# Performance work log

Measured on AMD Instinct MI355X. Metric: run time of the kernel, lower is better.

The kernel has to match this reference:

```python
import jax, jax.numpy as jnp
import numpy as np

C = 256
C8 = C // 8


def setup_inputs() -> dict:
    key = jax.random.key(0)
    ks = jax.random.split(key, 8)
    B, H, W = 4, 64, 64
    s = 0.05
    return {
        "x": jax.random.normal(ks[0], (B, C, H, W), jnp.float32),
        "Wq": jax.random.normal(ks[1], (C8, C), jnp.float32) * s,
        "bq": jax.random.normal(ks[2], (C8,), jnp.float32) * s,
        "Wk": jax.random.normal(ks[3], (C8, C), jnp.float32) * s,
        "bk": jax.random.normal(ks[4], (C8,), jnp.float32) * s,
        "Wv": jax.random.normal(ks[5], (C, C), jnp.float32) * s,
        "bv": jax.random.normal(ks[6], (C,), jnp.float32) * s,
        "gamma": jnp.zeros((1,), jnp.float32),
    }


def reference(x, Wq, bq, Wk, bk, Wv, bv, gamma):
    B, Ch, H, W = x.shape
    N = H * W
    xf = x.reshape(B, Ch, N)  # [B,C,N]
    # 1x1 convs == channel-mixing matmuls
    q = jnp.einsum("oc,bcn->bon", Wq, xf) + bq[None, :, None]  # [B,C8,N]
    k = jnp.einsum("oc,bcn->bon", Wk, xf) + bk[None, :, None]  # [B,C8,N]
    v = jnp.einsum("oc,bcn->bon", Wv, xf) + bv[None, :, None]  # [B,C,N]
    # energy[b,i,j] = sum_c q[b,c,i] * k[b,c,j]  (unscaled, as in original)
    energy = jnp.einsum("bci,bcj->bij", q, k)  # [B,N,N]
    attention = jax.nn.softmax(energy, axis=-1)  # softmax over j
    # out[b,c,i] = sum_j v[b,c,j] * attention[b,i,j]
    out = jnp.einsum("bcj,bij->bci", v, attention).reshape(B, Ch, H, W)
    out = gamma[0] * out + x
    attention_map = attention[0]
    return out, attention_map
```

## Files before the change

kernel.cpp:

```cpp
#include <hip/hip_runtime.h>
#include <hip/hip_bf16.h>
#include <cstdint>
#include <cstddef>

#define C_    256
#define C8_   32
#define NPIX  4096
#define BATCH 4
#define OUT_ELEMS (BATCH * C_ * NPIX)

typedef short bf16x8 __attribute__((ext_vector_type(8)));
typedef float f32x4  __attribute__((ext_vector_type(4)));
typedef unsigned uint32x2 __attribute__((ext_vector_type(2)));

#define LOG2E 1.44269504088896340736f

#define PROW 520

static __device__ __forceinline__ unsigned short f2bf(float f) {
    union { float f; unsigned u; } v; v.f = f;
    unsigned r = v.u + 0x7fff + ((v.u >> 16) & 1);
    return (unsigned short)(r >> 16);
}

static __device__ __forceinline__ unsigned pack_bf2(float p0, float p1) {
    union { float f; unsigned u; } a, b; a.f = p0; b.f = p1;
    return __builtin_amdgcn_perm(b.u, a.u, 0x07060302u);
}
static __device__ __forceinline__ float unpk_lo(unsigned u) {
    union { unsigned u; float f; } v; v.u = u << 16; return v.f;
}
static __device__ __forceinline__ float unpk_hi(unsigned u) {
    union { unsigned u; float f; } v; v.u = u & 0xffff0000u; return v.f;
}

static __device__ __forceinline__ f32x4 mfma16(bf16x8 a, bf16x8 b, f32x4 c) {
    return __builtin_amdgcn_mfma_f32_16x16x32_bf16(a, b, c, 0, 0, 0);
}

__global__ __launch_bounds__(256) void k_pre(
    const float* __restrict__ x,
    const float* __restrict__ Wq, const float* __restrict__ bq,
    const float* __restrict__ Wk, const float* __restrict__ bk,
    const float* __restrict__ Wv, const float* __restrict__ bv,
    const float* __restrict__ gamma,
    float* __restrict__ out,
    unsigned short* __restrict__ qT,
    unsigned short* __restrict__ kT,
    unsigned short* __restrict__ vB)
{
    __shared__ float xs[256][64];
    __shared__ float pred[4][8][64];

    const int bid = blockIdx.x;
    const float gval = gamma[0];

    if (bid >= 2048) {
        const size_t base = (size_t)(bid - 2048) * 256 + threadIdx.x;
        const f32x4* src = (const f32x4*)x;
        f32x4* dst = (f32x4*)out;
        f32x4 a = src[base];
        f32x4 b = src[base + 524288];
        __builtin_nontemporal_store(a, dst + base);
        __builtin_nontemporal_store(b, dst + base + 524288);
        return;
    }

    const int b   = bid >> 9;
    if (gval == 0.0f && b > 0) return;
    const int sub  = bid & 511;
    const int og8  = sub >> 6;
    const int n0   = (sub & 63) * 64;
    const bool is_q = (og8 < 4);
    const int obase = (og8 & 3) * 8;

    const int tl = threadIdx.x & 15;
    const int tr = threadIdx.x >> 4;
    const float* xb = x + (size_t)b * C_ * NPIX + n0;
    f32x4 v[16];
#pragma unroll
    for (int p = 0; p < 16; ++p)
        v[p] = *(const f32x4*)(xb + (size_t)(p * 16 + tr) * NPIX + tl * 4);
#pragma unroll
    for (int p = 0; p < 16; ++p)
        *(f32x4*)&xs[p * 16 + tr][tl * 4] = v[p];
    __syncthreads();

    const int wv = __builtin_amdgcn_readfirstlane(threadIdx.x >> 6);
    const int ln = threadIdx.x & 63;
    const float* Wb = (is_q ? Wq : Wk);
    float acc[8] = {0.f, 0.f, 0.f, 0.f, 0.f, 0.f, 0.f, 0.f};
#pragma unroll 8
    for (int cc = 0; cc < 64; ++cc) {
        const int c = wv * 64 + cc;
        const float xv = xs[c][ln];
#pragma unroll
        for (int o = 0; o < 8; ++o)
            acc[o] = fmaf(Wb[(size_t)(obase + o) * C_ + c], xv, acc[o]);
    }
#pragma unroll
    for (int o = 0; o < 8; ++o) pred[wv][o][ln] = acc[o];
    __syncthreads();

    const int o1 = threadIdx.x >> 6;
    const int n  = threadIdx.x & 63;
#pragma unroll
    for (int k = 0; k < 2; ++k) {
        const int ol = o1 + k * 4;
        const int oa = obase + ol;
        float s = pred[0][ol][n] + pred[1][ol][n] +
                  pred[2][ol][n] + pred[3][ol][n];
        if (is_q) {
            s = (s + bq[oa]) * LOG2E;
            qT[((size_t)b * NPIX + n0 + n) * C8_ + oa] = f2bf(s);
        } else {
            s = s + bk[oa];
            kT[((size_t)b * NPIX + n0 + n) * C8_ + oa] = f2bf(s);
        }
    }

    if (gval != 0.0f) {
        for (int ch = 0; ch < 4; ++ch) {
            const int vb0 = og8 * 32 + ch * 8;
            float vacc[8] = {0.f, 0.f, 0.f, 0.f, 0.f, 0.f, 0.f, 0.f};
#pragma unroll 8
            for (int cc = 0; cc < 64; ++cc) {
                const int c = wv * 64 + cc;
                const float xv = xs[c][ln];
#pragma unroll
                for (int o = 0; o < 8; ++o)
                    vacc[o] = fmaf(Wv[(size_t)(vb0 + o) * C_ + c], xv, vacc[o]);
            }
            __syncthreads();
#pragma unroll
            for (int o = 0; o < 8; ++o) pred[wv][o][ln] = vacc[o];
            __syncthreads();
#pragma unroll
            for (int k = 0; k < 2; ++k) {
                const int ol = o1 + k * 4;
                const int oa = vb0 + ol;
                float s = pred[0][ol][n] + pred[1][ol][n] +
                          pred[2][ol][n] + pred[3][ol][n] + bv[oa];
                vB[((size_t)b * C_ + oa) * NPIX + n0 + n] = f2bf(s);
            }
        }
    }
}

__global__ __launch_bounds__(512) void k_attn6(
    const float* __restrict__ x,
    const unsigned short* __restrict__ qT,
    const unsigned short* __restrict__ kT,
    const unsigned short* __restrict__ vB,
    const float* __restrict__ gamma,
    float* __restrict__ out,
    float* __restrict__ attn)
{
    const int b = blockIdx.y;
    const float g = gamma[0];
    if (g == 0.0f && b > 0) return;

    const int i0   = blockIdx.x * 16;
    const int t    = threadIdx.x;
    const int lane = t & 63;
    const int wavei = __builtin_amdgcn_readfirstlane(t >> 6);
    const int li   = lane & 15;
    const int lg   = lane >> 4;

    __shared__ unsigned short pbuf[8 * 16 * PROW];
    __shared__ float red[8][16];

    const unsigned short* qTb = qT + (size_t)b * NPIX * C8_;
    const unsigned short* kTb = kT + (size_t)b * NPIX * C8_;

    bf16x8 qf = *(const bf16x8*)(qTb + (size_t)(i0 + li) * C8_ + lg * 8);

    const int jw = wavei * 512;
    unsigned short* prow = pbuf + (size_t)(wavei * 16 + li) * PROW;

    float ssum = 0.f;
#pragma unroll
    for (int s = 0; s < 32; ++s) {
        bf16x8 kf = *(const bf16x8*)(kTb + (size_t)(jw + s * 16 + li) * C8_ + lg * 8);
        f32x4 z = {0.f, 0.f, 0.f, 0.f};
        f32x4 e = mfma16(kf, qf, z);
        float p0 = exp2f(e[0]);
        float p1 = exp2f(e[1]);
        float p2 = exp2f(e[2]);
        float p3 = exp2f(e[3]);
        ssum += (p0 + p1) + (p2 + p3);
        uint32x2 pk;
        pk.x = pack_bf2(p0, p1);
        pk.y = pack_bf2(p2, p3);
        *(uint32x2*)(prow + s * 16 + lg * 4) = pk;
    }

    ssum += __shfl_xor(ssum, 16, 64);
    ssum += __shfl_xor(ssum, 32, 64);
    if (lane < 16) red[wavei][lane] = ssum;
    __syncthreads();
    float l = 0.f;
#pragma unroll
    for (int w = 0; w < 8; ++w) l += red[w][li];
    const float inv = 1.0f / l;

    if (b == 0) {
#pragma unroll
        for (int r = 0; r < 16; ++r) {
            const float inv_r = __shfl(inv, r, 64);
            const unsigned short* rp = pbuf + (size_t)(wavei * 16 + r) * PROW;
            float* ap = attn + (size_t)(i0 + r) * NPIX + jw;
            uint32x2 u0 = *(const uint32x2*)(rp + lane * 4);
            uint32x2 u1 = *(const uint32x2*)(rp + 256 + lane * 4);
            f32x4 v0, v1;
            v0[0] = unpk_lo(u0.x) * inv_r; v0[1] = unpk_hi(u0.x) * inv_r;
            v0[2] = unpk_lo(u0.y) * inv_r; v0[3] = unpk_hi(u0.y) * inv_r;
            v1[0] = unpk_lo(u1.x) * inv_r; v1[1] = unpk_hi(u1.x) * inv_r;
            v1[2] = unpk_lo(u1.y) * inv_r; v1[3] = unpk_hi(u1.y) * inv_r;
            __builtin_nontemporal_store(v0, (f32x4*)(ap + lane * 4));
            __builtin_nontemporal_store(v1, (f32x4*)(ap + 256 + lane * 4));
        }
    }

    if (g != 0.0f) {
        f32x4 o0 = {0.f, 0.f, 0.f, 0.f};
        f32x4 o1 = {0.f, 0.f, 0.f, 0.f};
        const unsigned short* vb = vB + (size_t)b * C_ * NPIX;
        for (int st = 0; st < 8; ++st) {
            const int jbase = st * 512;
#pragma unroll
            for (int ks = 0; ks < 16; ++ks) {
                bf16x8 af = *(const bf16x8*)(pbuf + (size_t)(st * 16 + li) * PROW +
                                             ks * 32 + lg * 8);
                const unsigned short* vp0 =
                    vb + (size_t)(wavei * 32 + li) * NPIX + jbase + ks * 32 + lg * 8;
                bf16x8 vf0 = *(const bf16x8*)vp0;
                o0 = mfma16(af, vf0, o0);
                bf16x8 vf1 = *(const bf16x8*)(vp0 + (size_t)16 * NPIX);
                o1 = mfma16(af, vf1, o1);
            }
        }
        const float* xbt = x + (size_t)b * C_ * NPIX;
        float* outb = out + (size_t)b * C_ * NPIX;
        f32x4 sc;
#pragma unroll
        for (int r = 0; r < 4; ++r) sc[r] = g * __shfl(inv, lg * 4 + r, 64);
        {
            int c = wavei * 32 + li;
            f32x4 xv = *(const f32x4*)(xbt + (size_t)c * NPIX + i0 + lg * 4);
            f32x4 r0 = o0 * sc + xv;
            *(f32x4*)(outb + (size_t)c * NPIX + i0 + lg * 4) = r0;
            c += 16;
            f32x4 xv1 = *(const f32x4*)(xbt + (size_t)c * NPIX + i0 + lg * 4);
            f32x4 r1 = o1 * sc + xv1;
            *(f32x4*)(outb + (size_t)c * NPIX + i0 + lg * 4) = r1;
        }
    }
}

extern "C" void kernel_launch(void* const* d_in, const int* in_sizes, int n_in,
                              void* d_out, int out_size, void* d_ws, size_t ws_size,
                              hipStream_t stream) {
    (void)in_sizes; (void)n_in; (void)out_size; (void)ws_size;
    const float* x     = (const float*)d_in[0];
    const float* Wq    = (const float*)d_in[1];
    const float* bq    = (const float*)d_in[2];
    const float* Wk    = (const float*)d_in[3];
    const float* bk    = (const float*)d_in[4];
    const float* Wv    = (const float*)d_in[5];
    const float* bv    = (const float*)d_in[6];
    const float* gamma = (const float*)d_in[7];

    float* out  = (float*)d_out;
    float* attn = out + OUT_ELEMS;

    unsigned short* qT = (unsigned short*)d_ws;
    unsigned short* kT = qT + (size_t)BATCH * NPIX * C8_;
    unsigned short* vB = kT + (size_t)BATCH * NPIX * C8_;

    k_pre<<<4096, 256, 0, stream>>>(x, Wq, bq, Wk, bk, Wv, bv, gamma,
                                    out, qT, kT, vB);

    dim3 g2(NPIX / 16, BATCH);
    k_attn6<<<g2, 512, 0, stream>>>(x, qT, kT, vB, gamma, out, attn);
}
```

Before: 34.75 us.

## Move output copy into idle attention blocks and write full attention rows per wave

The x-to-out residual copy is removed from the preprocessing kernel. Attention blocks for batches 1-3, which exit early when gamma is zero, now perform it, so the copy overlaps with batch-0 attention instead of occupying the first kernel. The attention-map store is also reorganised so that each wave writes two complete contiguous rows rather than one 512-column segment of all 16 rows. The cost is a grid-stride copy loop that is valid only in the gamma-zero branch, and LDS reads that now span all segments.

```diff
diff --git a/kernel.cpp b/kernel.cpp
--- a/kernel.cpp
+++ b/kernel.cpp
@@ -44,7 +44,6 @@
     const float* __restrict__ Wk, const float* __restrict__ bk,
     const float* __restrict__ Wv, const float* __restrict__ bv,
     const float* __restrict__ gamma,
-    float* __restrict__ out,
     unsigned short* __restrict__ qT,
     unsigned short* __restrict__ kT,
     unsigned short* __restrict__ vB)
@@ -54,17 +53,6 @@
 
     const int bid = blockIdx.x;
     const float gval = gamma[0];
-
-    if (bid >= 2048) {
-        const size_t base = (size_t)(bid - 2048) * 256 + threadIdx.x;
-        const f32x4* src = (const f32x4*)x;
-        f32x4* dst = (f32x4*)out;
-        f32x4 a = src[base];
-        f32x4 b = src[base + 524288];
-        __builtin_nontemporal_store(a, dst + base);
-        __builtin_nontemporal_store(b, dst + base + 524288);
-        return;
-    }
 
     const int b   = bid >> 9;
     if (gval == 0.0f && b > 0) return;
@@ -147,7 +135,7 @@
     }
 }
 
-__global__ __launch_bounds__(512) void k_attn6(
+__global__ __launch_bounds__(512) void k_attn7(
     const float* __restrict__ x,
     const unsigned short* __restrict__ qT,
     const unsigned short* __restrict__ kT,
@@ -158,7 +146,20 @@
 {
     const int b = blockIdx.y;
     const float g = gamma[0];
-    if (g == 0.0f && b > 0) return;
+
+    __shared__ unsigned short pbuf[8 * 16 * PROW];
+    __shared__ float red[8][16];
+
+    if (g == 0.0f && b > 0) {
+        const int cb = (b - 1) * 256 + blockIdx.x;
+        const size_t n4 = (size_t)OUT_ELEMS / 4;
+        const f32x4* src = (const f32x4*)x;
+        f32x4* dst = (f32x4*)out;
+        for (size_t i = (size_t)cb * 512 + threadIdx.x; i < n4;
+             i += (size_t)768 * 512)
+            __builtin_nontemporal_store(src[i], dst + i);
+        return;
+    }
 
     const int i0   = blockIdx.x * 16;
     const int t    = threadIdx.x;
@@ -166,9 +167,6 @@
     const int wavei = __builtin_amdgcn_readfirstlane(t >> 6);
     const int li   = lane & 15;
     const int lg   = lane >> 4;
-
-    __shared__ unsigned short pbuf[8 * 16 * PROW];
-    __shared__ float red[8][16];
 
     const unsigned short* qTb = qT + (size_t)b * NPIX * C8_;
     const unsigned short* kTb = kT + (size_t)b * NPIX * C8_;
@@ -206,19 +204,25 @@
 
     if (b == 0) {
 #pragma unroll
-        for (int r = 0; r < 16; ++r) {
+        for (int rr = 0; rr < 2; ++rr) {
+            const int r = wavei * 2 + rr;
             const float inv_r = __shfl(inv, r, 64);
-            const unsigned short* rp = pbuf + (size_t)(wavei * 16 + r) * PROW;
-            float* ap = attn + (size_t)(i0 + r) * NPIX + jw;
-            uint32x2 u0 = *(const uint32x2*)(rp + lane * 4);
-            uint32x2 u1 = *(const uint32x2*)(rp + 256 + lane * 4);
-            f32x4 v0, v1;
-            v0[0] = unpk_lo(u0.x) * inv_r; v0[1] = unpk_hi(u0.x) * inv_r;
-            v0[2] = unpk_lo(u0.y) * inv_r; v0[3] = unpk_hi(u0.y) * inv_r;
-            v1[0] = unpk_lo(u1.x) * inv_r; v1[1] = unpk_hi(u1.x) * inv_r;
-            v1[2] = unpk_lo(u1.y) * inv_r; v1[3] = unpk_hi(u1.y) * inv_r;
-            __builtin_nontemporal_store(v0, (f32x4*)(ap + lane * 4));
-            __builtin_nontemporal_store(v1, (f32x4*)(ap + 256 + lane * 4));
+            float* rowp = attn + (size_t)(i0 + r) * NPIX;
+#pragma unroll
+            for (int seg = 0; seg < 8; ++seg) {
+                const unsigned short* rp = pbuf + (size_t)(seg * 16 + r) * PROW;
+                uint32x2 u0 = *(const uint32x2*)(rp + lane * 4);
+                uint32x2 u1 = *(const uint32x2*)(rp + 256 + lane * 4);
+                f32x4 v0, v1;
+                v0[0] = unpk_lo(u0.x) * inv_r; v0[1] = unpk_hi(u0.x) * inv_r;
+                v0[2] = unpk_lo(u0.y) * inv_r; v0[3] = unpk_hi(u0.y) * inv_r;
+                v1[0] = unpk_lo(u1.x) * inv_r; v1[1] = unpk_hi(u1.x) * inv_r;
+                v1[2] = unpk_lo(u1.y) * inv_r; v1[3] = unpk_hi(u1.y) * inv_r;
+                __builtin_nontemporal_store(
+                    v0, (f32x4*)(rowp + seg * 512 + lane * 4));
+                __builtin_nontemporal_store(
+                    v1, (f32x4*)(rowp + seg * 512 + 256 + lane * 4));
+            }
         }
     }
 
@@ -278,9 +282,9 @@
     unsigned short* kT = qT + (size_t)BATCH * NPIX * C8_;
     unsigned short* vB = kT + (size_t)BATCH * NPIX * C8_;
 
-    k_pre<<<4096, 256, 0, stream>>>(x, Wq, bq, Wk, bk, Wv, bv, gamma,
-                                    out, qT, kT, vB);
+    k_pre<<<2048, 256, 0, stream>>>(x, Wq, bq, Wk, bk, Wv, bv, gamma,
+                                    qT, kT, vB);
 
     dim3 g2(NPIX / 16, BATCH);
-    k_attn6<<<g2, 512, 0, stream>>>(x, qT, kT, vB, gamma, out, attn);
-}
+    k_attn7<<<g2, 512, 0, stream>>>(x, qT, kT, vB, gamma, out, attn);
+}
```

Result: faster. 33.02 us (-5.0%).
